# Kernel tuning notes

Measured on AMD Instinct MI355X. Metric: run time of the kernel, lower is better.

The kernel has to match this reference:

```python
import jax, jax.numpy as jnp
from jax import lax
import numpy as np

H = 2048
LX = 32
LY = 32


def setup_inputs() -> dict:
    key = jax.random.key(0)
    ks = jax.random.split(key, 9)
    N = LX * LY
    s = 1.0 / np.sqrt(H).astype(np.float32)
    inp = {
        "x": jax.random.normal(ks[0], (N,), jnp.float32),
        # embed: Dense(1 -> H)
        "We": jax.random.normal(ks[1], (1, H), jnp.float32),
        "be": jnp.zeros((H,), jnp.float32),
        # GRUCell input gates (with bias)
        "Wir": jax.random.normal(ks[2], (H, H), jnp.float32) * s,
        "bir": jnp.zeros((H,), jnp.float32),
        "Wiz": jax.random.normal(ks[3], (H, H), jnp.float32) * s,
        "biz": jnp.zeros((H,), jnp.float32),
        "Win": jax.random.normal(ks[4], (H, H), jnp.float32) * s,
        "bin_": jnp.zeros((H,), jnp.float32),
        # GRUCell recurrent gates (hr/hz bias-free, hn with bias, as in flax)
        "Whr": jax.random.normal(ks[5], (H, H), jnp.float32) * s,
        "Whz": jax.random.normal(ks[6], (H, H), jnp.float32) * s,
        "Whn": jax.random.normal(ks[7], (H, H), jnp.float32) * s,
        "bhn": jnp.zeros((H,), jnp.float32),
        "Lx": LX,
        "Ly": LY,
    }
    return inp


def snake_order(Lx: int, Ly: int):
    idx = np.arange(Lx * Ly).reshape(Ly, Lx)
    idx[1::2] = idx[1::2, ::-1]  # reverse odd rows -> snake pattern
    return jnp.asarray(idx.reshape(-1))


def reference(x, We, be, Wir, bir, Wiz, biz, Win, bin_, Whr, Whz, Whn, bhn, Lx, Ly):
    order = snake_order(Lx, Ly)                      # (N,) visit order
    # embed each scalar site value: Dense(1->H), vectorized over all sites
    xe = x[order][:, None] * We[0][None, :] + be     # (N, H)
    # precompute input-gate projections for all steps (same math, batched)
    a_r = xe @ Wir + bir                             # (N, H)
    a_z = xe @ Wiz + biz
    a_n = xe @ Win + bin_
    h0 = jnp.zeros((Whr.shape[0],), xe.dtype)

    def step(h, g):
        ar, az, an = g
        r = jax.nn.sigmoid(ar + h @ Whr)
        z = jax.nn.sigmoid(az + h @ Whz)
        n = jnp.tanh(an + r * (h @ Whn + bhn))
        h_new = (1.0 - z) * n + z * h
        return h_new, None

    h, _ = lax.scan(step, h0, (a_r, a_z, a_n))
    return h
```

## Files before the change

kernel.cpp:

```cpp
#include <hip/hip_runtime.h>

#define HDIM 2048
#define TSTEPS 1024
#define NBLK 256
#define NTHR 512
#define CPB 8
#define TAGM 0x3FFu

typedef unsigned long long ull;

__device__ __forceinline__ int snake_src(int t) {
    int y = t >> 5, p = t & 31;
    return (y & 1) ? (y * 32 + 31 - p) : t;
}
__device__ __forceinline__ float sigmoid_f(float v) {
    return __builtin_amdgcn_rcpf(1.f + __expf(-v));
}
__device__ __forceinline__ float tanh_f(float v) {
    return 1.f - 2.f * __builtin_amdgcn_rcpf(__expf(2.f * v) + 1.f);
}

__global__ __launch_bounds__(NTHR, 2) void gru_all(
    const float* __restrict__ x,
    const float* __restrict__ We,  const float* __restrict__ be,
    const float* __restrict__ Wir, const float* __restrict__ bir,
    const float* __restrict__ Wiz, const float* __restrict__ biz,
    const float* __restrict__ Win, const float* __restrict__ bin_,
    const float* __restrict__ Whr, const float* __restrict__ Whz,
    const float* __restrict__ Whn, const float* __restrict__ bhn,
    float* __restrict__ out, unsigned* __restrict__ u0, unsigned* __restrict__ u1)
{
    const int tid  = threadIdx.x;
    const int blk  = blockIdx.x;
    const int c    = tid & 7;
    const int r    = tid >> 3;
    const int col  = blk * CPB + c;
    const int row0 = r * 32;
    const int lane = tid & 63, wv = tid >> 6;

    __shared__ __align__(16) float lds_h[2304];
    __shared__ float sBe[HDIM];
    __shared__ float red[8][6][8];

    for (int i = tid; i < HDIM; i += NTHR) { lds_h[i] = We[i]; sBe[i] = be[i]; }
    __syncthreads();

    float wr[32], wz[32], wn[32];
#pragma unroll
    for (int k = 0; k < 32; ++k) {
        size_t off = (size_t)(row0 + k) * HDIM + col;
        wr[k] = Whr[off];
        wz[k] = Whz[off];
        wn[k] = Whn[off];
    }

    float eR=0,eZ=0,eN=0,bRa=0,bZa=0,bNa=0;
#pragma unroll 8
    for (int k = 0; k < 32; ++k) {
        size_t off = (size_t)(row0 + k) * HDIM + col;
        float we = lds_h[row0 + k], bb = sBe[row0 + k];
        float w0 = Wir[off], w1 = Wiz[off], w2 = Win[off];
        eR  = fmaf(we, w0, eR);  bRa = fmaf(bb, w0, bRa);
        eZ  = fmaf(we, w1, eZ);  bZa = fmaf(bb, w1, bZa);
        eN  = fmaf(we, w2, eN);  bNa = fmaf(bb, w2, bNa);
    }
#pragma unroll
    for (int m = 8; m < 64; m <<= 1) {
        eR  += __shfl_xor(eR,  m, 64); eZ  += __shfl_xor(eZ,  m, 64);
        eN  += __shfl_xor(eN,  m, 64); bRa += __shfl_xor(bRa, m, 64);
        bZa += __shfl_xor(bZa, m, 64); bNa += __shfl_xor(bNa, m, 64);
    }
    if (lane < 8) {
        red[wv][0][lane]=eR;  red[wv][1][lane]=eZ;  red[wv][2][lane]=eN;
        red[wv][3][lane]=bRa; red[wv][4][lane]=bZa; red[wv][5][lane]=bNa;
    }
    __syncthreads();

    float vrc=0,vzc=0,vnc=0,crc=0,czc=0,cnc=0,bhc=0;
    if (tid < 8) {
#pragma unroll
        for (int w = 0; w < 8; ++w) {
            vrc += red[w][0][tid]; vzc += red[w][1][tid]; vnc += red[w][2][tid];
            crc += red[w][3][tid]; czc += red[w][4][tid]; cnc += red[w][5][tid];
        }
        crc += bir[col]; czc += biz[col]; cnc += bin_[col];
        bhc = bhn[col];

        float x0 = x[snake_src(0)];
        float ar = fmaf(x0, vrc, crc);
        float az = fmaf(x0, vzc, czc);
        float an = fmaf(x0, vnc, cnc);
        float rg = sigmoid_f(ar), zg = sigmoid_f(az);
        float ng = tanh_f(fmaf(rg, bhc, an));
        float h1 = (1.f - zg) * ng;
        unsigned pk = (__float_as_uint(h1) & ~TAGM) | 1u;
        __hip_atomic_store(&u1[col], pk, __ATOMIC_RELAXED, __HIP_MEMORY_SCOPE_AGENT);
    }

    const int sbase = tid * 4;
    const int lwb   = sbase + ((sbase >> 6) << 2);
    const int lrb   = row0  + ((row0  >> 6) << 2);
    const int pcol  = col + ((col >> 6) << 2);

    for (int t = 1; t < TSTEPS; ++t) {
        const unsigned* sin  = (t & 1) ? u1 : u0;
        unsigned*       sout = (t & 1) ? u0 : u1;
        const unsigned  tg   = (unsigned)t & TAGM;

        const ull* pp = (const ull*)sin + 2 * tid;
        ull v0, v1;
        for (;;) {
            v0 = __hip_atomic_load(&pp[0], __ATOMIC_RELAXED, __HIP_MEMORY_SCOPE_AGENT);
            v1 = __hip_atomic_load(&pp[1], __ATOMIC_RELAXED, __HIP_MEMORY_SCOPE_AGENT);
            unsigned a = (unsigned)v0, b = (unsigned)(v0 >> 32);
            unsigned d = (unsigned)v1, e = (unsigned)(v1 >> 32);
            if ((a & TAGM) == tg && (b & TAGM) == tg &&
                (d & TAGM) == tg && (e & TAGM) == tg) break;
        }
        float4 hq = make_float4(__uint_as_float((unsigned)v0        & ~TAGM),
                                __uint_as_float((unsigned)(v0 >> 32) & ~TAGM),
                                __uint_as_float((unsigned)v1        & ~TAGM),
                                __uint_as_float((unsigned)(v1 >> 32) & ~TAGM));
        *(float4*)&lds_h[lwb] = hq;
        __syncthreads();

        float a0 = 0.f, a1 = 0.f, a2 = 0.f;
#pragma unroll
        for (int k = 0; k < 32; ++k) {
            float hv = lds_h[lrb + k];
            a0 = fmaf(hv, wr[k], a0);
            a1 = fmaf(hv, wz[k], a1);
            a2 = fmaf(hv, wn[k], a2);
        }
#pragma unroll
        for (int m = 8; m < 64; m <<= 1) {
            a0 += __shfl_xor(a0, m, 64);
            a1 += __shfl_xor(a1, m, 64);
            a2 += __shfl_xor(a2, m, 64);
        }
        if (lane < 8) { red[wv][0][lane]=a0; red[wv][1][lane]=a1; red[wv][2][lane]=a2; }
        __syncthreads();

        if (tid < 8) {
            float Sr=0, Sz=0, Sn=0;
#pragma unroll
            for (int w = 0; w < 8; ++w) {
                Sr += red[w][0][tid]; Sz += red[w][1][tid]; Sn += red[w][2][tid];
            }
            float xt = x[snake_src(t)];
            float ar = fmaf(xt, vrc, crc) + Sr;
            float az = fmaf(xt, vzc, czc) + Sz;
            float an = fmaf(xt, vnc, cnc);
            float rg = sigmoid_f(ar), zg = sigmoid_f(az);
            float ng = tanh_f(an + rg * (Sn + bhc));
            float hold = lds_h[pcol];
            float hnew = (1.f - zg) * ng + zg * hold;
            if (t == TSTEPS - 1) {
                out[col] = hnew;
            } else {
                unsigned pk = (__float_as_uint(hnew) & ~TAGM) | ((unsigned)(t + 1) & TAGM);
                __hip_atomic_store(&sout[col], pk, __ATOMIC_RELAXED, __HIP_MEMORY_SCOPE_AGENT);
            }
        }
        __syncthreads();
    }
}

extern "C" void kernel_launch(void* const* d_in, const int* in_sizes, int n_in,
                              void* d_out, int out_size, void* d_ws, size_t ws_size,
                              hipStream_t stream) {
    const float* x    = (const float*)d_in[0];
    const float* We   = (const float*)d_in[1];
    const float* be   = (const float*)d_in[2];
    const float* Wir  = (const float*)d_in[3];
    const float* bir  = (const float*)d_in[4];
    const float* Wiz  = (const float*)d_in[5];
    const float* biz  = (const float*)d_in[6];
    const float* Win  = (const float*)d_in[7];
    const float* bin_ = (const float*)d_in[8];
    const float* Whr  = (const float*)d_in[9];
    const float* Whz  = (const float*)d_in[10];
    const float* Whn  = (const float*)d_in[11];
    const float* bhn  = (const float*)d_in[12];

    unsigned* u0 = (unsigned*)d_ws;
    unsigned* u1 = u0 + HDIM;

    gru_all<<<NBLK, NTHR, 0, stream>>>(x, We, be, Wir, bir, Wiz, biz, Win, bin_,
                                       Whr, Whz, Whn, bhn,
                                       (float*)d_out, u0, u1);
}
```

Baseline: 2.555 ms.

## Assign one wavefront per column, reducing via shuffles and dropping block barriers

The work split changes so each wavefront owns one output column and covers all 2048 rows with lane-strided float4 LDS reads. The cross-wave LDS reduction and two of the three per-step __syncthreads go away: the shuffle reduction spans the full wave and every lane computes the gate math redundantly. The h buffer in LDS is double-buffered so one barrier per step suffices. The snake-ordered x is staged in LDS, and the packed-tag mantissa truncation now rounds (+512). The cost is redundant gate math per wave and a different LDS access pattern.

```diff
diff --git a/kernel.cpp b/kernel.cpp
--- a/kernel.cpp
+++ b/kernel.cpp
@@ -4,7 +4,6 @@
 #define TSTEPS 1024
 #define NBLK 256
 #define NTHR 512
-#define CPB 8
 #define TAGM 0x3FFu
 
 typedef unsigned long long ull;
@@ -32,137 +31,123 @@
 {
     const int tid  = threadIdx.x;
     const int blk  = blockIdx.x;
-    const int c    = tid & 7;
-    const int r    = tid >> 3;
-    const int col  = blk * CPB + c;
-    const int row0 = r * 32;
-    const int lane = tid & 63, wv = tid >> 6;
+    const int lane = tid & 63;
+    const int wv   = tid >> 6;
+    const int col  = blk * 8 + wv;
 
-    __shared__ __align__(16) float lds_h[2304];
-    __shared__ float sBe[HDIM];
-    __shared__ float red[8][6][8];
+    __shared__ __align__(16) float hb[2][HDIM];
+    __shared__ float sX[TSTEPS];
 
-    for (int i = tid; i < HDIM; i += NTHR) { lds_h[i] = We[i]; sBe[i] = be[i]; }
-    __syncthreads();
+    for (int i = tid; i < TSTEPS; i += NTHR) sX[i] = x[snake_src(i)];
 
     float wr[32], wz[32], wn[32];
 #pragma unroll
-    for (int k = 0; k < 32; ++k) {
-        size_t off = (size_t)(row0 + k) * HDIM + col;
-        wr[k] = Whr[off];
-        wz[k] = Whz[off];
-        wn[k] = Whn[off];
+    for (int k = 0; k < 8; ++k) {
+#pragma unroll
+        for (int j = 0; j < 4; ++j) {
+            size_t off = (size_t)(k * 256 + lane * 4 + j) * HDIM + col;
+            wr[k * 4 + j] = Whr[off];
+            wz[k * 4 + j] = Whz[off];
+            wn[k * 4 + j] = Whn[off];
+        }
     }
 
-    float eR=0,eZ=0,eN=0,bRa=0,bZa=0,bNa=0;
-#pragma unroll 8
+    float eR = 0, eZ = 0, eN = 0, bR = 0, bZ = 0, bN = 0;
+#pragma unroll 4
     for (int k = 0; k < 32; ++k) {
-        size_t off = (size_t)(row0 + k) * HDIM + col;
-        float we = lds_h[row0 + k], bb = sBe[row0 + k];
+        int row = k * 64 + lane;
+        float we = We[row], bb = be[row];
+        size_t off = (size_t)row * HDIM + col;
         float w0 = Wir[off], w1 = Wiz[off], w2 = Win[off];
-        eR  = fmaf(we, w0, eR);  bRa = fmaf(bb, w0, bRa);
-        eZ  = fmaf(we, w1, eZ);  bZa = fmaf(bb, w1, bZa);
-        eN  = fmaf(we, w2, eN);  bNa = fmaf(bb, w2, bNa);
+        eR = fmaf(we, w0, eR);  bR = fmaf(bb, w0, bR);
+        eZ = fmaf(we, w1, eZ);  bZ = fmaf(bb, w1, bZ);
+        eN = fmaf(we, w2, eN);  bN = fmaf(bb, w2, bN);
     }
 #pragma unroll
-    for (int m = 8; m < 64; m <<= 1) {
-        eR  += __shfl_xor(eR,  m, 64); eZ  += __shfl_xor(eZ,  m, 64);
-        eN  += __shfl_xor(eN,  m, 64); bRa += __shfl_xor(bRa, m, 64);
-        bZa += __shfl_xor(bZa, m, 64); bNa += __shfl_xor(bNa, m, 64);
+    for (int m = 1; m < 64; m <<= 1) {
+        eR += __shfl_xor(eR, m, 64); eZ += __shfl_xor(eZ, m, 64);
+        eN += __shfl_xor(eN, m, 64); bR += __shfl_xor(bR, m, 64);
+        bZ += __shfl_xor(bZ, m, 64); bN += __shfl_xor(bN, m, 64);
     }
-    if (lane < 8) {
-        red[wv][0][lane]=eR;  red[wv][1][lane]=eZ;  red[wv][2][lane]=eN;
-        red[wv][3][lane]=bRa; red[wv][4][lane]=bZa; red[wv][5][lane]=bNa;
-    }
+    const float vrc = eR, vzc = eZ, vnc = eN;
+    const float crc = bR + bir[col];
+    const float czc = bZ + biz[col];
+    const float cnc = bN + bin_[col];
+    const float bhc = bhn[col];
+
     __syncthreads();
 
-    float vrc=0,vzc=0,vnc=0,crc=0,czc=0,cnc=0,bhc=0;
-    if (tid < 8) {
-#pragma unroll
-        for (int w = 0; w < 8; ++w) {
-            vrc += red[w][0][tid]; vzc += red[w][1][tid]; vnc += red[w][2][tid];
-            crc += red[w][3][tid]; czc += red[w][4][tid]; cnc += red[w][5][tid];
-        }
-        crc += bir[col]; czc += biz[col]; cnc += bin_[col];
-        bhc = bhn[col];
-
-        float x0 = x[snake_src(0)];
+    {
+        float x0 = sX[0];
         float ar = fmaf(x0, vrc, crc);
         float az = fmaf(x0, vzc, czc);
         float an = fmaf(x0, vnc, cnc);
         float rg = sigmoid_f(ar), zg = sigmoid_f(az);
         float ng = tanh_f(fmaf(rg, bhc, an));
         float h1 = (1.f - zg) * ng;
-        unsigned pk = (__float_as_uint(h1) & ~TAGM) | 1u;
-        __hip_atomic_store(&u1[col], pk, __ATOMIC_RELAXED, __HIP_MEMORY_SCOPE_AGENT);
+        if (lane == 0) {
+            unsigned pk = ((__float_as_uint(h1) + 512u) & ~TAGM) | 1u;
+            __hip_atomic_store(&u1[col], pk, __ATOMIC_RELAXED, __HIP_MEMORY_SCOPE_AGENT);
+        }
     }
 
-    const int sbase = tid * 4;
-    const int lwb   = sbase + ((sbase >> 6) << 2);
-    const int lrb   = row0  + ((row0  >> 6) << 2);
-    const int pcol  = col + ((col >> 6) << 2);
+    const ull M2 = 0x000003FF000003FFull;
 
     for (int t = 1; t < TSTEPS; ++t) {
-        const unsigned* sin  = (t & 1) ? u1 : u0;
-        unsigned*       sout = (t & 1) ? u0 : u1;
+        const unsigned* pin  = (t & 1) ? u1 : u0;
+        unsigned*       pout = (t & 1) ? u0 : u1;
         const unsigned  tg   = (unsigned)t & TAGM;
+        const ull       tg2  = ((ull)tg << 32) | (ull)tg;
 
-        const ull* pp = (const ull*)sin + 2 * tid;
+        const ull* pp = (const ull*)pin + 2 * tid;
         ull v0, v1;
         for (;;) {
             v0 = __hip_atomic_load(&pp[0], __ATOMIC_RELAXED, __HIP_MEMORY_SCOPE_AGENT);
             v1 = __hip_atomic_load(&pp[1], __ATOMIC_RELAXED, __HIP_MEMORY_SCOPE_AGENT);
-            unsigned a = (unsigned)v0, b = (unsigned)(v0 >> 32);
-            unsigned d = (unsigned)v1, e = (unsigned)(v1 >> 32);
-            if ((a & TAGM) == tg && (b & TAGM) == tg &&
-                (d & TAGM) == tg && (e & TAGM) == tg) break;
+            if (!(((v0 ^ tg2) | (v1 ^ tg2)) & M2)) break;
         }
-        float4 hq = make_float4(__uint_as_float((unsigned)v0        & ~TAGM),
+        float* hc = hb[t & 1];
+        float4 hq = make_float4(__uint_as_float((unsigned)v0         & ~TAGM),
                                 __uint_as_float((unsigned)(v0 >> 32) & ~TAGM),
-                                __uint_as_float((unsigned)v1        & ~TAGM),
+                                __uint_as_float((unsigned)v1         & ~TAGM),
                                 __uint_as_float((unsigned)(v1 >> 32) & ~TAGM));
-        *(float4*)&lds_h[lwb] = hq;
+        *(float4*)&hc[tid * 4] = hq;
         __syncthreads();
+
+        float hold = hc[col];
+        float xt   = sX[t];
 
         float a0 = 0.f, a1 = 0.f, a2 = 0.f;
 #pragma unroll
-        for (int k = 0; k < 32; ++k) {
-            float hv = lds_h[lrb + k];
-            a0 = fmaf(hv, wr[k], a0);
-            a1 = fmaf(hv, wz[k], a1);
-            a2 = fmaf(hv, wn[k], a2);
+        for (int k = 0; k < 8; ++k) {
+            float4 h4 = *(const float4*)&hc[k * 256 + lane * 4];
+            a0 = fmaf(h4.x, wr[k*4+0], a0); a1 = fmaf(h4.x, wz[k*4+0], a1); a2 = fmaf(h4.x, wn[k*4+0], a2);
+            a0 = fmaf(h4.y, wr[k*4+1], a0); a1 = fmaf(h4.y, wz[k*4+1], a1); a2 = fmaf(h4.y, wn[k*4+1], a2);
+            a0 = fmaf(h4.z, wr[k*4+2], a0); a1 = fmaf(h4.z, wz[k*4+2], a1); a2 = fmaf(h4.z, wn[k*4+2], a2);
+            a0 = fmaf(h4.w, wr[k*4+3], a0); a1 = fmaf(h4.w, wz[k*4+3], a1); a2 = fmaf(h4.w, wn[k*4+3], a2);
         }
+
 #pragma unroll
-        for (int m = 8; m < 64; m <<= 1) {
+        for (int m = 1; m < 64; m <<= 1) {
             a0 += __shfl_xor(a0, m, 64);
             a1 += __shfl_xor(a1, m, 64);
             a2 += __shfl_xor(a2, m, 64);
         }
-        if (lane < 8) { red[wv][0][lane]=a0; red[wv][1][lane]=a1; red[wv][2][lane]=a2; }
-        __syncthreads();
 
-        if (tid < 8) {
-            float Sr=0, Sz=0, Sn=0;
-#pragma unroll
-            for (int w = 0; w < 8; ++w) {
-                Sr += red[w][0][tid]; Sz += red[w][1][tid]; Sn += red[w][2][tid];
-            }
-            float xt = x[snake_src(t)];
-            float ar = fmaf(xt, vrc, crc) + Sr;
-            float az = fmaf(xt, vzc, czc) + Sz;
-            float an = fmaf(xt, vnc, cnc);
-            float rg = sigmoid_f(ar), zg = sigmoid_f(az);
-            float ng = tanh_f(an + rg * (Sn + bhc));
-            float hold = lds_h[pcol];
-            float hnew = (1.f - zg) * ng + zg * hold;
-            if (t == TSTEPS - 1) {
-                out[col] = hnew;
-            } else {
-                unsigned pk = (__float_as_uint(hnew) & ~TAGM) | ((unsigned)(t + 1) & TAGM);
-                __hip_atomic_store(&sout[col], pk, __ATOMIC_RELAXED, __HIP_MEMORY_SCOPE_AGENT);
-            }
+        float ar = fmaf(xt, vrc, crc) + a0;
+        float az = fmaf(xt, vzc, czc) + a1;
+        float an = fmaf(xt, vnc, cnc);
+        float rg = sigmoid_f(ar), zg = sigmoid_f(az);
+        float ng = tanh_f(an + rg * (a2 + bhc));
+        float hnew = (1.f - zg) * ng + zg * hold;
+
+        if (t == TSTEPS - 1) {
+            if (lane == 0) out[col] = hnew;
+        } else if (lane == 0) {
+            unsigned pk = ((__float_as_uint(hnew) + 512u) & ~TAGM)
+                        | ((unsigned)(t + 1) & TAGM);
+            __hip_atomic_store(&pout[col], pk, __ATOMIC_RELAXED, __HIP_MEMORY_SCOPE_AGENT);
         }
-        __syncthreads();
     }
 }
 
```

Measured after the change: 5.495 ms. +115.1%, slower.

## Double-buffer LDS state to drop trailing barrier and precompute next input gates

Applied to the files above, without the earlier changes.

Splits the hidden-state buffer and the reduction scratch into two parity-indexed copies, which lets the final __syncthreads of each step be removed. The snake-ordered x is preloaded into LDS, and the next step's input-gate values are computed right after the state is published. The cross-wave reduction now uses wave-shuffles in wave 0 instead of a serial loop, and the tag check is folded into 64-bit masks. Tagged values are rounded (+512) rather than truncated. The cost is more LDS use and a reliance on parity buffering for correctness.

```diff
diff --git a/kernel.cpp b/kernel.cpp
--- a/kernel.cpp
+++ b/kernel.cpp
@@ -38,11 +38,12 @@
     const int row0 = r * 32;
     const int lane = tid & 63, wv = tid >> 6;
 
-    __shared__ __align__(16) float lds_h[2304];
-    __shared__ float sBe[HDIM];
-    __shared__ float red[8][6][8];
-
-    for (int i = tid; i < HDIM; i += NTHR) { lds_h[i] = We[i]; sBe[i] = be[i]; }
+    __shared__ __align__(16) float hb[2][2176];
+    __shared__ float red[2][8][3][8];
+    __shared__ float sX[TSTEPS];
+
+    for (int i = tid; i < HDIM; i += NTHR) { hb[0][i] = We[i]; hb[1][i] = be[i]; }
+    for (int i = tid; i < TSTEPS; i += NTHR) sX[i] = x[snake_src(i)];
     __syncthreads();
 
     float wr[32], wz[32], wn[32];
@@ -58,7 +59,7 @@
 #pragma unroll 8
     for (int k = 0; k < 32; ++k) {
         size_t off = (size_t)(row0 + k) * HDIM + col;
-        float we = lds_h[row0 + k], bb = sBe[row0 + k];
+        float we = hb[0][row0 + k], bb = hb[1][row0 + k];
         float w0 = Wir[off], w1 = Wiz[off], w2 = Win[off];
         eR  = fmaf(we, w0, eR);  bRa = fmaf(bb, w0, bRa);
         eZ  = fmaf(we, w1, eZ);  bZa = fmaf(bb, w1, bZa);
@@ -71,63 +72,73 @@
         bZa += __shfl_xor(bZa, m, 64); bNa += __shfl_xor(bNa, m, 64);
     }
     if (lane < 8) {
-        red[wv][0][lane]=eR;  red[wv][1][lane]=eZ;  red[wv][2][lane]=eN;
-        red[wv][3][lane]=bRa; red[wv][4][lane]=bZa; red[wv][5][lane]=bNa;
+        red[0][wv][0][lane]=eR;  red[0][wv][1][lane]=eZ;  red[0][wv][2][lane]=eN;
+        red[1][wv][0][lane]=bRa; red[1][wv][1][lane]=bZa; red[1][wv][2][lane]=bNa;
     }
     __syncthreads();
 
     float vrc=0,vzc=0,vnc=0,crc=0,czc=0,cnc=0,bhc=0;
+    float aR=0, aZ=0, aN=0;
     if (tid < 8) {
 #pragma unroll
         for (int w = 0; w < 8; ++w) {
-            vrc += red[w][0][tid]; vzc += red[w][1][tid]; vnc += red[w][2][tid];
-            crc += red[w][3][tid]; czc += red[w][4][tid]; cnc += red[w][5][tid];
+            vrc += red[0][w][0][tid]; vzc += red[0][w][1][tid]; vnc += red[0][w][2][tid];
+            crc += red[1][w][0][tid]; czc += red[1][w][1][tid]; cnc += red[1][w][2][tid];
         }
         crc += bir[col]; czc += biz[col]; cnc += bin_[col];
         bhc = bhn[col];
 
-        float x0 = x[snake_src(0)];
+        float x0 = sX[0];
         float ar = fmaf(x0, vrc, crc);
         float az = fmaf(x0, vzc, czc);
         float an = fmaf(x0, vnc, cnc);
         float rg = sigmoid_f(ar), zg = sigmoid_f(az);
         float ng = tanh_f(fmaf(rg, bhc, an));
         float h1 = (1.f - zg) * ng;
-        unsigned pk = (__float_as_uint(h1) & ~TAGM) | 1u;
+        unsigned pk = ((__float_as_uint(h1) + 512u) & ~TAGM) | 1u;
         __hip_atomic_store(&u1[col], pk, __ATOMIC_RELAXED, __HIP_MEMORY_SCOPE_AGENT);
+
+        float x1 = sX[1];
+        aR = fmaf(x1, vrc, crc);
+        aZ = fmaf(x1, vzc, czc);
+        aN = fmaf(x1, vnc, cnc);
     }
 
     const int sbase = tid * 4;
     const int lwb   = sbase + ((sbase >> 6) << 2);
     const int lrb   = row0  + ((row0  >> 6) << 2);
-    const int pcol  = col + ((col >> 6) << 2);
+    const int pcol  = col   + ((col   >> 6) << 2);
+    const ull  M2   = 0x000003FF000003FFull;
 
     for (int t = 1; t < TSTEPS; ++t) {
-        const unsigned* sin  = (t & 1) ? u1 : u0;
-        unsigned*       sout = (t & 1) ? u0 : u1;
+        const int par = t & 1;
+        const unsigned* pin  = par ? u1 : u0;
+        unsigned*       pout = par ? u0 : u1;
         const unsigned  tg   = (unsigned)t & TAGM;
-
-        const ull* pp = (const ull*)sin + 2 * tid;
+        const ull       tg2  = ((ull)tg << 32) | (ull)tg;
+
+        const ull* pp = (const ull*)pin + 2 * tid;
         ull v0, v1;
         for (;;) {
             v0 = __hip_atomic_load(&pp[0], __ATOMIC_RELAXED, __HIP_MEMORY_SCOPE_AGENT);
             v1 = __hip_atomic_load(&pp[1], __ATOMIC_RELAXED, __HIP_MEMORY_SCOPE_AGENT);
-            unsigned a = (unsigned)v0, b = (unsigned)(v0 >> 32);
-            unsigned d = (unsigned)v1, e = (unsigned)(v1 >> 32);
-            if ((a & TAGM) == tg && (b & TAGM) == tg &&
-                (d & TAGM) == tg && (e & TAGM) == tg) break;
-        }
-        float4 hq = make_float4(__uint_as_float((unsigned)v0        & ~TAGM),
+            if (!(((v0 ^ tg2) | (v1 ^ tg2)) & M2)) break;
+        }
+        float* hc = hb[par];
+        float4 hq = make_float4(__uint_as_float((unsigned)v0         & ~TAGM),
                                 __uint_as_float((unsigned)(v0 >> 32) & ~TAGM),
-                                __uint_as_float((unsigned)v1        & ~TAGM),
+                                __uint_as_float((unsigned)v1         & ~TAGM),
                                 __uint_as_float((unsigned)(v1 >> 32) & ~TAGM));
-        *(float4*)&lds_h[lwb] = hq;
+        *(float4*)&hc[lwb] = hq;
         __syncthreads();
 
+        float hold = 0.f;
+        if (wv == 0) hold = hc[pcol];
+
         float a0 = 0.f, a1 = 0.f, a2 = 0.f;
 #pragma unroll
         for (int k = 0; k < 32; ++k) {
-            float hv = lds_h[lrb + k];
+            float hv = hc[lrb + k];
             a0 = fmaf(hv, wr[k], a0);
             a1 = fmaf(hv, wz[k], a1);
             a2 = fmaf(hv, wn[k], a2);
@@ -138,31 +149,40 @@
             a1 += __shfl_xor(a1, m, 64);
             a2 += __shfl_xor(a2, m, 64);
         }
-        if (lane < 8) { red[wv][0][lane]=a0; red[wv][1][lane]=a1; red[wv][2][lane]=a2; }
+        if (lane < 8) { red[par][wv][0][lane]=a0; red[par][wv][1][lane]=a1; red[par][wv][2][lane]=a2; }
         __syncthreads();
 
-        if (tid < 8) {
-            float Sr=0, Sz=0, Sn=0;
-#pragma unroll
-            for (int w = 0; w < 8; ++w) {
-                Sr += red[w][0][tid]; Sz += red[w][1][tid]; Sn += red[w][2][tid];
+        if (wv == 0) {
+            const int w  = lane >> 3, cc = lane & 7;
+            float s0 = red[par][w][0][cc];
+            float s1 = red[par][w][1][cc];
+            float s2 = red[par][w][2][cc];
+#pragma unroll
+            for (int m = 8; m < 64; m <<= 1) {
+                s0 += __shfl_xor(s0, m, 64);
+                s1 += __shfl_xor(s1, m, 64);
+                s2 += __shfl_xor(s2, m, 64);
             }
-            float xt = x[snake_src(t)];
-            float ar = fmaf(xt, vrc, crc) + Sr;
-            float az = fmaf(xt, vzc, czc) + Sz;
-            float an = fmaf(xt, vnc, cnc);
-            float rg = sigmoid_f(ar), zg = sigmoid_f(az);
-            float ng = tanh_f(an + rg * (Sn + bhc));
-            float hold = lds_h[pcol];
-            float hnew = (1.f - zg) * ng + zg * hold;
-            if (t == TSTEPS - 1) {
-                out[col] = hnew;
-            } else {
-                unsigned pk = (__float_as_uint(hnew) & ~TAGM) | ((unsigned)(t + 1) & TAGM);
-                __hip_atomic_store(&sout[col], pk, __ATOMIC_RELAXED, __HIP_MEMORY_SCOPE_AGENT);
+            if (lane < 8) {
+                float ar = aR + s0;
+                float az = aZ + s1;
+                float an = aN;
+                float rg = sigmoid_f(ar), zg = sigmoid_f(az);
+                float ng = tanh_f(an + rg * (s2 + bhc));
+                float hnew = (1.f - zg) * ng + zg * hold;
+                if (t == TSTEPS - 1) {
+                    out[col] = hnew;
+                } else {
+                    unsigned pk = ((__float_as_uint(hnew) + 512u) & ~TAGM)
+                                | ((unsigned)(t + 1) & TAGM);
+                    __hip_atomic_store(&pout[col], pk, __ATOMIC_RELAXED, __HIP_MEMORY_SCOPE_AGENT);
+                    float xn = sX[t + 1];
+                    aR = fmaf(xn, vrc, crc);
+                    aZ = fmaf(xn, vzc, czc);
+                    aN = fmaf(xn, vnc, cnc);
+                }
             }
         }
-        __syncthreads();
     }
 }
 
```

New measurement: 2.884 ms. +12.9%, slower.
